# Kernel optimization log

Measured on AMD Instinct MI355X. Metric: run time of the kernel, lower is better.

Reference implementation:

```python
import math
import jax, jax.numpy as jnp
import numpy as np

B, C, F, W_FRAMES = 1, 8, 1024, 512
H = 16                      # num_heads
D = F // H                  # head dim = 64
ROPE_DIM = D // 2           # 32: only first half of head dim is rotated
EXP = 4                     # ffn expansion
EPS = 1e-5
MAX_FREQ = 10.0             # rotary-embedding-torch default


def frame_norm(x, g, b):
    # LayerNorm over the feature axis (axis=2) of (b, c, F, w)
    mu = jnp.mean(x, axis=2, keepdims=True)
    var = jnp.mean(jnp.square(x - mu), axis=2, keepdims=True)
    xn = (x - mu) * jax.lax.rsqrt(var + EPS)
    return xn * g[None, None, :, None] + b[None, None, :, None]


def mc_linear(x, w_pw):
    # per-channel pointwise linear: out[b,c,f,w] = sum_g W[c,f,g] x[b,c,g,w]
    return jnp.einsum('bcgw,cfg->bcfw', x, w_pw)


def apply_rope(t, freqs_seq):
    # t: (b, c, H, w, d); freqs_seq: (w, rot_dim)
    rot_dim = freqs_seq.shape[-1]
    t_rot, t_pass = t[..., :rot_dim], t[..., rot_dim:]
    cos, sin = jnp.cos(freqs_seq), jnp.sin(freqs_seq)
    x1, x2 = t_rot[..., 0::2], t_rot[..., 1::2]
    rh = jnp.stack([-x2, x1], axis=-1).reshape(t_rot.shape)  # interleaved rotate_half
    return jnp.concatenate([t_rot * cos + rh * sin, t_pass], axis=-1)


def attention(x, w_q, w_o, rope_freqs):
    b, c, f, w = x.shape
    # NOTE: source uses q_proj for q, k AND v (k_proj/v_proj unused)
    p = mc_linear(x, w_q)                                    # (b,c,F,w)
    t = p.transpose(0, 1, 3, 2).reshape(b, c, w, H, D).transpose(0, 1, 3, 2, 4)  # (b,c,H,w,d)
    pos = jnp.arange(w, dtype=t.dtype)
    freqs_seq = jnp.repeat(pos[:, None] * rope_freqs[None, :], 2, axis=-1)  # (w, rot_dim)
    q = apply_rope(t, freqs_seq)
    k = apply_rope(t, freqs_seq)
    v = t
    scores = jnp.einsum('bchqd,bchkd->bchqk', q, k) / math.sqrt(f)  # scaled by sqrt(features)!
    a = jax.nn.softmax(scores, axis=-1)
    o = jnp.einsum('bchqk,bchkd->bchqd', a, v)
    o = o.transpose(0, 1, 3, 2, 4).reshape(b, c, w, f).transpose(0, 1, 3, 2)  # (b,c,F,w)
    return mc_linear(o, w_o)


def setup_inputs() -> dict:
    key = jax.random.key(0)
    ks = jax.random.split(key, 8)
    s = 1.0 / math.sqrt(F)
    se = 1.0 / math.sqrt(F * EXP)
    x = jax.random.normal(ks[0], (B, C, F, W_FRAMES), dtype=jnp.float32)
    w_q = jax.random.uniform(ks[1], (C, F, F), jnp.float32, -s, s)
    w_o = jax.random.uniform(ks[2], (C, F, F), jnp.float32, -s, s)
    w1 = jax.random.uniform(ks[3], (C, F * EXP, F), jnp.float32, -s, s)
    w2 = jax.random.uniform(ks[4], (C, F, F * EXP), jnp.float32, -se, se)
    rope_freqs = jnp.linspace(1.0, MAX_FREQ / 2, ROPE_DIM // 2, dtype=jnp.float32) * math.pi
    return {
        'x': x,
        'norm1_g': jnp.ones((F,), jnp.float32), 'norm1_b': jnp.zeros((F,), jnp.float32),
        'w_q': w_q, 'w_o': w_o, 'rope_freqs': rope_freqs,
        'norm2_g': jnp.ones((F,), jnp.float32), 'norm2_b': jnp.zeros((F,), jnp.float32),
        'w1': w1, 'w2': w2,
    }


def reference(x, norm1_g, norm1_b, w_q, w_o, rope_freqs, norm2_g, norm2_b, w1, w2):
    # FrameTransformerEncoder, eval mode (dropout = identity)
    z = frame_norm(x, norm1_g, norm1_b)
    x = x + attention(z, w_q, w_o, rope_freqs)
    z = frame_norm(x, norm2_g, norm2_b)
    z = mc_linear(jax.nn.gelu(mc_linear(z, w1), approximate=False), w2)
    return x + z
```

## Files before the change

kernel.cpp:

```cpp
#include <hip/hip_runtime.h>
#include <math.h>

#define CC 8
#define FF 1024
#define WW 512
#define HH 16
#define DD 64
#define FE 4096
#define EPS_ 1e-5f

typedef __attribute__((ext_vector_type(8))) short bf16x8;
typedef __attribute__((ext_vector_type(4))) float f32x4;

static __device__ __forceinline__ unsigned short f2bf(float f) {
    unsigned u = __float_as_uint(f);
    u += 0x7fffu + ((u >> 16) & 1u);
    return (unsigned short)(u >> 16);
}
static __device__ __forceinline__ float bf2f(unsigned short h) {
    return __uint_as_float(((unsigned)h) << 16);
}
static __device__ __forceinline__ float gelu_exact(float v) {
    return 0.5f * v * (1.0f + erff(v * 0.70710678118654752f));
}
static __device__ __forceinline__ unsigned cvt_pk_bf16(float lo, float hi) {
    unsigned r;
    asm("v_cvt_pk_bf16_f32 %0, %1, %2" : "=v"(r) : "v"(lo), "v"(hi));
    return r;
}

typedef const __attribute__((address_space(1))) unsigned int* gas_p;
typedef __attribute__((address_space(3))) unsigned int* las_p;
static __device__ __forceinline__ void gload_lds16(const void* g, void* l) {
    __builtin_amdgcn_global_load_lds((gas_p)g, (las_p)l, 16, 0, 0);
}

__global__ __launch_bounds__(256) void fn_stats_k(
    const float* __restrict__ x, float2* __restrict__ part)
{
    int c  = blockIdx.z;
    int w0 = blockIdx.x * 64;
    int f0 = blockIdx.y * 128;
    int t  = threadIdx.x, wl = t & 63, fg = t >> 6;
    const float* xc = x + (size_t)c * FF * WW;

    float s = 0.f, q = 0.f;
    #pragma unroll 8
    for (int i = 0; i < 32; i++) {
        int f = f0 + fg + 4 * i;
        float v = xc[(size_t)f * WW + w0 + wl];
        s += v; q += v * v;
    }
    __shared__ float ss[4][64], sq_[4][64];
    ss[fg][wl] = s; sq_[fg][wl] = q;
    __syncthreads();
    if (fg == 0) {
        float S = 0.f, Q = 0.f;
        #pragma unroll
        for (int j = 0; j < 4; j++) { S += ss[j][wl]; Q += sq_[j][wl]; }
        part[((size_t)c * WW + w0 + wl) * 8 + blockIdx.y] = make_float2(S, Q);
    }
}

__global__ __launch_bounds__(256) void fn_apply_k(
    const float* __restrict__ x, const float2* __restrict__ part,
    const float* __restrict__ g, const float* __restrict__ b,
    unsigned short* __restrict__ zt)
{
    int c  = blockIdx.z;
    int w0 = blockIdx.x * 64;
    int f0 = blockIdx.y * 64;
    int t  = threadIdx.x, wl = t & 63, fg = t >> 6;

    __shared__ float smu[64], srv[64];
    __shared__ float sT[64][65];

    if (t < 64) {
        float S = 0.f, Q = 0.f;
        #pragma unroll
        for (int fs = 0; fs < 8; fs++) {
            float2 v = part[((size_t)c * WW + w0 + t) * 8 + fs];
            S += v.x; Q += v.y;
        }
        float mu  = S * (1.f / FF);
        float var = Q * (1.f / FF) - mu * mu;
        smu[t] = mu;
        srv[t] = rsqrtf(var + EPS_);
    }
    const float* xc = x + (size_t)c * FF * WW;
    #pragma unroll
    for (int i = 0; i < 16; i++) {
        int fl = fg * 16 + i;
        sT[fl][wl] = xc[(size_t)(f0 + fl) * WW + w0 + wl];
    }
    __syncthreads();

    unsigned short* ztc = zt + (size_t)c * WW * FF;
    float gv = g[f0 + wl], bv = b[f0 + wl];
    #pragma unroll
    for (int i = 0; i < 16; i++) {
        int wr = fg * 16 + i;
        ztc[(size_t)(w0 + wr) * FF + f0 + wl] =
            f2bf((sT[wl][wr] - smu[wr]) * srv[wr] * gv + bv);
    }
}

template<int BM, int MINW>
__global__ __launch_bounds__(256, MINW) void gemm_v6_k(
    const float* __restrict__ A, const unsigned short* __restrict__ Bt,
    float* __restrict__ Outf, unsigned short* __restrict__ Outb,
    const float* __restrict__ Add, int M, int K, int mode)
{
    constexpr int L  = BM / 16;
    constexpr int MI = BM / 32;
    constexpr int AP = 72;

    int bid = blockIdx.x;
    int c   = bid & 7;
    int rem = bid >> 3;
    int nt  = rem & 3;
    int mt  = rem >> 2;
    int m0  = mt * BM, n0 = nt * 128;
    const float*          Ac = A  + (size_t)c * M * K;
    const unsigned short* Bc = Bt + ((size_t)c * 512 + n0) * K;

    __shared__ unsigned short sA[2][BM * AP];
    __shared__ unsigned short sB[2][128 * 64];

    int t    = threadIdx.x;
    int lane = t & 63;
    int wid  = t >> 6;
    int frl  = lane & 15, fgr = lane >> 4;
    int WM   = (wid >> 1) * (MI * 16);
    int WN   = (wid & 1) * 64;

    f32x4 acc[MI][4];
    #pragma unroll
    for (int i = 0; i < MI; i++)
        #pragma unroll
        for (int j = 0; j < 4; j++) acc[i][j] = (f32x4){0.f, 0.f, 0.f, 0.f};

    int arow = t >> 4;
    int acol = (t & 15) * 4;
    float4 ar[L];

    int bro   = lane >> 3;
    int bslot = (lane & 7) ^ bro;

    auto loadA = [&](int k0) {
        #pragma unroll
        for (int p = 0; p < L; p++)
            ar[p] = *reinterpret_cast<const float4*>(
                Ac + (size_t)(m0 + p * 16 + arow) * K + k0 + acol);
    };
    auto cvtWriteA = [&](int buf) {
        #pragma unroll
        for (int p = 0; p < L; p++) {
            uint2 u;
            u.x = cvt_pk_bf16(ar[p].x, ar[p].y);
            u.y = cvt_pk_bf16(ar[p].z, ar[p].w);
            *reinterpret_cast<uint2*>(&sA[buf][(p * 16 + arow) * AP + acol]) = u;
        }
    };
    auto stageB = [&](int buf, int k0) {
        #pragma unroll
        for (int r = 0; r < 4; r++) {
            int rbase = wid * 32 + r * 8;
            gload_lds16(Bc + (size_t)(rbase + bro) * K + k0 + bslot * 8,
                        &sB[buf][rbase * 64]);
        }
    };

    loadA(0);
    asm volatile("s_waitcnt vmcnt(0)" ::: "memory");
    cvtWriteA(0);
    stageB(0, 0);

    int NT = K >> 6;
    for (int kt = 0; kt < NT; ++kt) {
        int  cur  = kt & 1;
        bool more = (kt + 1 < NT);

        if (more) loadA((kt + 1) << 6);
        if (more) {
            if constexpr (BM == 128)
                asm volatile("s_waitcnt vmcnt(8)" ::: "memory");
            else
                asm volatile("s_waitcnt vmcnt(4)" ::: "memory");
        } else {
            asm volatile("s_waitcnt vmcnt(0)" ::: "memory");
        }
        asm volatile("s_waitcnt lgkmcnt(0)" ::: "memory");
        __builtin_amdgcn_sched_barrier(0);
        __builtin_amdgcn_s_barrier();

        if (more) stageB(cur ^ 1, (kt + 1) << 6);

        #pragma unroll
        for (int ks = 0; ks < 2; ks++) {
            bf16x8 af[MI], bfv[4];
            #pragma unroll
            for (int mi = 0; mi < MI; mi++)
                af[mi] = *reinterpret_cast<const bf16x8*>(
                    &sA[cur][(WM + mi * 16 + frl) * AP + ks * 32 + fgr * 8]);
            #pragma unroll
            for (int ni = 0; ni < 4; ni++) {
                int row  = WN + ni * 16 + frl;
                int slot = ((ks << 2) | fgr) ^ (frl & 7);
                bfv[ni] = *reinterpret_cast<const bf16x8*>(
                    &sB[cur][row * 64 + slot * 8]);
            }
            #pragma unroll
            for (int mi = 0; mi < MI; mi++)
                #pragma unroll
                for (int ni = 0; ni < 4; ni++)
                    acc[mi][ni] = __builtin_amdgcn_mfma_f32_16x16x32_bf16(
                        af[mi], bfv[ni], acc[mi][ni], 0, 0, 0);
        }

        if (more) {
            asm volatile("s_waitcnt vmcnt(4)" ::: "memory");
            __builtin_amdgcn_sched_barrier(0);
            cvtWriteA(cur ^ 1);
        }
    }

    if (mode == 1) {
        #pragma unroll
        for (int mi = 0; mi < MI; mi++)
            #pragma unroll
            for (int ni = 0; ni < 4; ni++) {
                int mrow = m0 + WM + mi * 16 + fgr * 4;
                int ncol = n0 + WN + ni * 16 + frl;
                #pragma unroll
                for (int r = 0; r < 4; r++) {
                    size_t o = ((size_t)c * M + mrow + r) * 512 + ncol;
                    Outf[o] = acc[mi][ni][r] + Add[o];
                }
            }
    } else {
        bool gel = (mode == 2);
        #pragma unroll
        for (int mi = 0; mi < MI; mi++)
            #pragma unroll
            for (int ni = 0; ni < 4; ni++) {
                f32x4 v = acc[mi][ni];
                if (gel) {
                    v[0] = gelu_exact(v[0]); v[1] = gelu_exact(v[1]);
                    v[2] = gelu_exact(v[2]); v[3] = gelu_exact(v[3]);
                }
                int mrow = m0 + WM + mi * 16 + fgr * 4;
                int ncol = n0 + WN + ni * 16 + frl;
                ushort4 h;
                h.x = f2bf(v[0]); h.y = f2bf(v[1]);
                h.z = f2bf(v[2]); h.w = f2bf(v[3]);
                *reinterpret_cast<ushort4*>(
                    &Outb[((size_t)c * 512 + ncol) * M + mrow]) = h;
            }
    }
}

__global__ __launch_bounds__(256, 2) void gemm_w1big_k(
    const float* __restrict__ A, const unsigned short* __restrict__ Bt,
    unsigned short* __restrict__ Outb, int M, int K)
{
    constexpr int L  = 4;
    constexpr int G  = 4;
    constexpr int AP = 40;

    int bid = blockIdx.x;
    int c   = bid & 7;
    int rem = bid >> 3;
    int nt  = rem & 1;
    int mt  = rem >> 1;
    int m0  = mt * 128, n0 = nt * 256;
    const float*          Ac = A  + (size_t)c * M * K;
    const unsigned short* Bc = Bt + ((size_t)c * 512 + n0) * K;

    __shared__ unsigned short sA[2][128 * AP];
    __shared__ unsigned short sB[2][256 * 32];

    int t    = threadIdx.x;
    int lane = t & 63;
    int wid  = t >> 6;
    int frl  = lane & 15, fgr = lane >> 4;
    int WM   = (wid >> 1) * 64;
    int WN   = (wid & 1) * 128;

    f32x4 acc[4][8];
    #pragma unroll
    for (int i = 0; i < 4; i++)
        #pragma unroll
        for (int j = 0; j < 8; j++) acc[i][j] = (f32x4){0.f, 0.f, 0.f, 0.f};

    int arow = t >> 3;
    int acol = (t & 7) * 4;
    float4 ar[L];

    int bro   = lane >> 2;
    int bslot = (lane & 3) ^ (bro & 3);

    auto loadA = [&](int k0) {
        #pragma unroll
        for (int p = 0; p < L; p++)
            ar[p] = *reinterpret_cast<const float4*>(
                Ac + (size_t)(m0 + p * 32 + arow) * K + k0 + acol);
    };
    auto cvtWriteA = [&](int buf) {
        #pragma unroll
        for (int p = 0; p < L; p++) {
            uint2 u;
            u.x = cvt_pk_bf16(ar[p].x, ar[p].y);
            u.y = cvt_pk_bf16(ar[p].z, ar[p].w);
            *reinterpret_cast<uint2*>(&sA[buf][(p * 32 + arow) * AP + acol]) = u;
        }
    };
    auto stageB = [&](int buf, int k0) {
        #pragma unroll
        for (int r = 0; r < G; r++) {
            int rbase = wid * 64 + r * 16;
            gload_lds16(Bc + (size_t)(rbase + bro) * K + k0 + bslot * 8,
                        &sB[buf][rbase * 32]);
        }
    };

    loadA(0);
    asm volatile("s_waitcnt vmcnt(0)" ::: "memory");
    cvtWriteA(0);
    stageB(0, 0);

    int NT = K >> 5;
    for (int kt = 0; kt < NT; ++kt) {
        int  cur  = kt & 1;
        bool more = (kt + 1 < NT);

        if (more) loadA((kt + 1) << 5);
        if (more)
            asm volatile("s_waitcnt vmcnt(4)" ::: "memory");
        else
            asm volatile("s_waitcnt vmcnt(0)" ::: "memory");
        asm volatile("s_waitcnt lgkmcnt(0)" ::: "memory");
        __builtin_amdgcn_sched_barrier(0);
        __builtin_amdgcn_s_barrier();

        if (more) stageB(cur ^ 1, (kt + 1) << 5);

        {
            bf16x8 af[4], bfv[8];
            #pragma unroll
            for (int mi = 0; mi < 4; mi++)
                af[mi] = *reinterpret_cast<const bf16x8*>(
                    &sA[cur][(WM + mi * 16 + frl) * AP + fgr * 8]);
            #pragma unroll
            for (int ni = 0; ni < 8; ni++) {
                int row  = WN + ni * 16 + frl;
                int slot = fgr ^ (row & 3);
                bfv[ni] = *reinterpret_cast<const bf16x8*>(
                    &sB[cur][row * 32 + slot * 8]);
            }
            #pragma unroll
            for (int mi = 0; mi < 4; mi++)
                #pragma unroll
                for (int ni = 0; ni < 8; ni++)
                    acc[mi][ni] = __builtin_amdgcn_mfma_f32_16x16x32_bf16(
                        af[mi], bfv[ni], acc[mi][ni], 0, 0, 0);
        }

        if (more) {
            asm volatile("s_waitcnt vmcnt(4)" ::: "memory");
            __builtin_amdgcn_sched_barrier(0);
            cvtWriteA(cur ^ 1);
        }
    }

    #pragma unroll
    for (int mi = 0; mi < 4; mi++)
        #pragma unroll
        for (int ni = 0; ni < 8; ni++) {
            f32x4 v = acc[mi][ni];
            v[0] = gelu_exact(v[0]); v[1] = gelu_exact(v[1]);
            v[2] = gelu_exact(v[2]); v[3] = gelu_exact(v[3]);
            int mrow = m0 + WM + mi * 16 + fgr * 4;
            int ncol = n0 + WN + ni * 16 + frl;
            ushort4 h;
            h.x = f2bf(v[0]); h.y = f2bf(v[1]);
            h.z = f2bf(v[2]); h.w = f2bf(v[3]);
            *reinterpret_cast<ushort4*>(
                &Outb[((size_t)c * 512 + ncol) * M + mrow]) = h;
        }
}

__global__ __launch_bounds__(256) void attn_mfma_k(
    const unsigned short* __restrict__ pt, const float* __restrict__ fr,
    unsigned short* __restrict__ ot)
{
    int ch = blockIdx.y;
    int c  = ch >> 4, h = ch & 15;
    int q0 = blockIdx.x * 64;
    int t  = threadIdx.x;
    int lane = t & 63;
    int wid  = t >> 6;
    int frl  = lane & 15, fgr = lane >> 4;

    const unsigned short* base = pt + (size_t)c * WW * FF + h * DD;

    __shared__ unsigned short Qs[64 * 72];
    __shared__ unsigned short Ks[64 * 72];
    __shared__ unsigned short Vt[64 * 72];
    __shared__ unsigned short Ps[4 * 16 * 72];

    {
        int kr = t >> 3, d0 = (t & 7) * 8;
        #pragma unroll
        for (int r = 0; r < 2; r++) {
            int row = kr + r * 32;
            int w   = q0 + row;
            bf16x8 v = *reinterpret_cast<const bf16x8*>(&base[(size_t)w * FF + d0]);
            bf16x8 o;
            if (d0 < 32) {
                #pragma unroll
                for (int j = 0; j < 8; j += 2) {
                    float x1 = bf2f((unsigned short)v[j]);
                    float x2 = bf2f((unsigned short)v[j + 1]);
                    float sn, cs;
                    __sincosf((float)w * fr[(d0 + j) >> 1], &sn, &cs);
                    o[j]     = (short)f2bf(x1 * cs - x2 * sn);
                    o[j + 1] = (short)f2bf(x2 * cs + x1 * sn);
                }
            } else o = v;
            *reinterpret_cast<bf16x8*>(&Qs[row * 72 + d0]) = o;
        }
    }

    f32x4 oacc[4];
    float m_[4], l_[4];
    #pragma unroll
    for (int i = 0; i < 4; i++) {
        oacc[i] = (f32x4){0.f, 0.f, 0.f, 0.f};
        m_[i] = -1e30f; l_[i] = 0.f;
    }
    unsigned short* myP = &Ps[wid * 16 * 72];
    int wq0 = wid * 16;

    for (int k0 = 0; k0 < WW; k0 += 64) {
        __syncthreads();
        {
            int kr = t >> 3, d0 = (t & 7) * 8;
            #pragma unroll
            for (int r = 0; r < 2; r++) {
                int row = kr + r * 32;
                int w   = k0 + row;
                bf16x8 v = *reinterpret_cast<const bf16x8*>(&base[(size_t)w * FF + d0]);
                bf16x8 o;
                if (d0 < 32) {
                    #pragma unroll
                    for (int j = 0; j < 8; j += 2) {
                        float x1 = bf2f((unsigned short)v[j]);
                        float x2 = bf2f((unsigned short)v[j + 1]);
                        float sn, cs;
                        __sincosf((float)w * fr[(d0 + j) >> 1], &sn, &cs);
                        o[j]     = (short)f2bf(x1 * cs - x2 * sn);
                        o[j + 1] = (short)f2bf(x2 * cs + x1 * sn);
                    }
                } else o = v;
                *reinterpret_cast<bf16x8*>(&Ks[row * 72 + d0]) = o;
            }
        }
        {
            int d  = t & 63;
            int kb = (t >> 6) * 8;
            #pragma unroll
            for (int r = 0; r < 2; r++) {
                int kk = kb + r * 32;
                bf16x8 o;
                #pragma unroll
                for (int j = 0; j < 8; j++)
                    o[j] = (short)base[(size_t)(k0 + kk + j) * FF + d];
                *reinterpret_cast<bf16x8*>(&Vt[d * 72 + kk]) = o;
            }
        }
        __syncthreads();

        f32x4 s[4];
        #pragma unroll
        for (int nt = 0; nt < 4; nt++) s[nt] = (f32x4){0.f, 0.f, 0.f, 0.f};
        bf16x8 aq0 = *reinterpret_cast<const bf16x8*>(&Qs[(wq0 + frl) * 72 + fgr * 8]);
        bf16x8 aq1 = *reinterpret_cast<const bf16x8*>(&Qs[(wq0 + frl) * 72 + 32 + fgr * 8]);
        #pragma unroll
        for (int nt = 0; nt < 4; nt++) {
            bf16x8 b0 = *reinterpret_cast<const bf16x8*>(&Ks[(nt * 16 + frl) * 72 + fgr * 8]);
            bf16x8 b1 = *reinterpret_cast<const bf16x8*>(&Ks[(nt * 16 + frl) * 72 + 32 + fgr * 8]);
            s[nt] = __builtin_amdgcn_mfma_f32_16x16x32_bf16(aq0, b0, s[nt], 0, 0, 0);
            s[nt] = __builtin_amdgcn_mfma_f32_16x16x32_bf16(aq1, b1, s[nt], 0, 0, 0);
        }

        #pragma unroll
        for (int r = 0; r < 4; r++) {
            float sv[4];
            #pragma unroll
            for (int nt = 0; nt < 4; nt++) sv[nt] = s[nt][r] * (1.f / 32.f);
            float mx = fmaxf(fmaxf(sv[0], sv[1]), fmaxf(sv[2], sv[3]));
            mx = fmaxf(mx, __shfl_xor(mx, 1, 64));
            mx = fmaxf(mx, __shfl_xor(mx, 2, 64));
            mx = fmaxf(mx, __shfl_xor(mx, 4, 64));
            mx = fmaxf(mx, __shfl_xor(mx, 8, 64));
            float mn    = fmaxf(m_[r], mx);
            float scale = __expf(m_[r] - mn);
            float rs = 0.f;
            #pragma unroll
            for (int nt = 0; nt < 4; nt++) {
                float p = __expf(sv[nt] - mn);
                myP[(fgr * 4 + r) * 72 + nt * 16 + frl] = f2bf(p);
                rs += p;
            }
            rs += __shfl_xor(rs, 1, 64);
            rs += __shfl_xor(rs, 2, 64);
            rs += __shfl_xor(rs, 4, 64);
            rs += __shfl_xor(rs, 8, 64);
            l_[r] = l_[r] * scale + rs;
            m_[r] = mn;
            #pragma unroll
            for (int dt = 0; dt < 4; dt++) oacc[dt][r] *= scale;
        }

        bf16x8 ap0 = *reinterpret_cast<const bf16x8*>(&myP[frl * 72 + fgr * 8]);
        bf16x8 ap1 = *reinterpret_cast<const bf16x8*>(&myP[frl * 72 + 32 + fgr * 8]);
        #pragma unroll
        for (int dt = 0; dt < 4; dt++) {
            bf16x8 b0 = *reinterpret_cast<const bf16x8*>(&Vt[(dt * 16 + frl) * 72 + fgr * 8]);
            bf16x8 b1 = *reinterpret_cast<const bf16x8*>(&Vt[(dt * 16 + frl) * 72 + 32 + fgr * 8]);
            oacc[dt] = __builtin_amdgcn_mfma_f32_16x16x32_bf16(ap0, b0, oacc[dt], 0, 0, 0);
            oacc[dt] = __builtin_amdgcn_mfma_f32_16x16x32_bf16(ap1, b1, oacc[dt], 0, 0, 0);
        }
    }

    unsigned short* ob = ot + (size_t)c * WW * FF + h * DD;
    #pragma unroll
    for (int r = 0; r < 4; r++) {
        float inv = 1.f / l_[r];
        int w = q0 + wq0 + fgr * 4 + r;
        #pragma unroll
        for (int dt = 0; dt < 4; dt++)
            ob[(size_t)w * FF + dt * 16 + frl] = f2bf(oacc[dt][r] * inv);
    }
}

extern "C" void kernel_launch(void* const* d_in, const int* in_sizes, int n_in,
                              void* d_out, int out_size, void* d_ws, size_t ws_size,
                              hipStream_t stream)
{
    const float* x  = (const float*)d_in[0];
    const float* g1 = (const float*)d_in[1];
    const float* b1 = (const float*)d_in[2];
    const float* wq = (const float*)d_in[3];
    const float* wo = (const float*)d_in[4];
    const float* fr = (const float*)d_in[5];
    const float* g2 = (const float*)d_in[6];
    const float* b2 = (const float*)d_in[7];
    const float* w1 = (const float*)d_in[8];
    const float* w2 = (const float*)d_in[9];

    const size_t SZ = (size_t)CC * FF * WW;
    char* wsb = (char*)d_ws;
    unsigned short* zt  = (unsigned short*)(wsb);
    unsigned short* ptb = (unsigned short*)(wsb + 2 * SZ);
    unsigned short* otb = (unsigned short*)(wsb + 4 * SZ);
    float*          x2  = (float*)        (wsb + 6 * SZ);
    unsigned short* h1t = (unsigned short*)(wsb + 10 * SZ);
    float2*         prt = (float2*)       (wsb + 18 * SZ);

    dim3 b256(256);
    dim3 gst(WW / 64, FF / 128, CC);
    dim3 gap(WW / 64, FF / 64, CC);

    fn_stats_k<<<gst, b256, 0, stream>>>(x, prt);
    fn_apply_k<<<gap, b256, 0, stream>>>(x, prt, g1, b1, zt);
    gemm_v6_k<64, 3><<<dim3(512), b256, 0, stream>>>(
        wq, zt, nullptr, ptb, nullptr, FF, FF, 0);
    attn_mfma_k<<<dim3(WW / 64, CC * HH), b256, 0, stream>>>(ptb, fr, otb);
    gemm_v6_k<64, 3><<<dim3(512), b256, 0, stream>>>(
        wo, otb, x2, nullptr, x, FF, FF, 1);
    fn_stats_k<<<gst, b256, 0, stream>>>(x2, prt);
    fn_apply_k<<<gap, b256, 0, stream>>>(x2, prt, g2, b2, zt);
    gemm_w1big_k<<<dim3(512), b256, 0, stream>>>(w1, zt, h1t, FE, FF);
    gemm_v6_k<64, 3><<<dim3(512), b256, 0, stream>>>(
        w2, h1t, (float*)d_out, nullptr, x2, FF, FE, 1);
}
```

Baseline: 259.9 us.

## Replace block-shared FFN GEMMs with barrier-free per-wave tiled GEMM kernel

The FFN GEMM kernels (w1 with GELU, and w2 with residual add) are replaced by a templated kernel in which each wave owns private LDS buffers for its A and B tiles. This removes the block-wide s_barrier per k-step and adds deeper A register prefetch, two tiles ahead. The w2 GEMM now uses this kernel in place of gemm_v6_k. The tradeoff is that B tiles are no longer shared across waves, so each wave loads its own B and global and LDS traffic rises. Smaller per-wave tiles also lower MFMA reuse per load.

```diff
diff --git a/kernel.cpp b/kernel.cpp
--- a/kernel.cpp
+++ b/kernel.cpp
@@ -260,134 +260,158 @@
     }
 }
 
-__global__ __launch_bounds__(256, 2) void gemm_w1big_k(
+template<int MI, int NI, int MODE>
+__global__ __launch_bounds__(256, 2) void gemm_wfree_k(
     const float* __restrict__ A, const unsigned short* __restrict__ Bt,
-    unsigned short* __restrict__ Outb, int M, int K)
+    float* __restrict__ Outf, unsigned short* __restrict__ Outb,
+    const float* __restrict__ Add, int M, int K)
 {
-    constexpr int L  = 4;
-    constexpr int G  = 4;
-    constexpr int AP = 40;
+    constexpr int R   = MI * 16;
+    constexpr int BN  = NI * 16;
+    constexpr int L   = R / 8;
+    constexpr int G   = NI;
+    constexpr int NTn = 512 / BN;
+    constexpr int LPR = 64 / R;
+    constexpr int FPL = 32 / LPR;
 
     int bid = blockIdx.x;
     int c   = bid & 7;
     int rem = bid >> 3;
-    int nt  = rem & 1;
-    int mt  = rem >> 1;
-    int m0  = mt * 128, n0 = nt * 256;
-    const float*          Ac = A  + (size_t)c * M * K;
-    const unsigned short* Bc = Bt + ((size_t)c * 512 + n0) * K;
-
-    __shared__ unsigned short sA[2][128 * AP];
-    __shared__ unsigned short sB[2][256 * 32];
+    int nt  = rem & (NTn - 1);
+    int mtb = rem / NTn;
 
     int t    = threadIdx.x;
     int lane = t & 63;
     int wid  = t >> 6;
+    int m0w  = (mtb * 4 + wid) * R;
+    int n0   = nt * BN;
+
+    const float*          Ac = A  + (size_t)c * M * K;
+    const unsigned short* Bc = Bt + ((size_t)c * 512 + n0) * K;
+
+    __shared__ unsigned short sB[4][BN * 32];
+    __shared__ unsigned short sA[4][2][R * 40];
+    unsigned short* sBw = sB[wid];
+
     int frl  = lane & 15, fgr = lane >> 4;
-    int WM   = (wid >> 1) * 64;
-    int WN   = (wid & 1) * 128;
-
-    f32x4 acc[4][8];
+    int arow = lane / LPR, asub = lane % LPR;
+    int bro  = lane >> 2;
+    int bslot = (lane & 3) ^ (bro & 3);
+
+    f32x4 acc[MI][NI];
     #pragma unroll
-    for (int i = 0; i < 4; i++)
-        #pragma unroll
-        for (int j = 0; j < 8; j++) acc[i][j] = (f32x4){0.f, 0.f, 0.f, 0.f};
-
-    int arow = t >> 3;
-    int acol = (t & 7) * 4;
-    float4 ar[L];
-
-    int bro   = lane >> 2;
-    int bslot = (lane & 3) ^ (bro & 3);
-
-    auto loadA = [&](int k0) {
+    for (int i = 0; i < MI; i++)
+        #pragma unroll
+        for (int j = 0; j < NI; j++) acc[i][j] = (f32x4){0.f, 0.f, 0.f, 0.f};
+
+    float4 ar0[L], ar1[L];
+
+    auto loadAinto = [&](int k0, float4 (&ar)[L]) {
         #pragma unroll
         for (int p = 0; p < L; p++)
             ar[p] = *reinterpret_cast<const float4*>(
-                Ac + (size_t)(m0 + p * 32 + arow) * K + k0 + acol);
+                Ac + (size_t)(m0w + arow) * K + k0 + asub * FPL + p * 4);
     };
-    auto cvtWriteA = [&](int buf) {
+    auto cvtWriteA = [&](int buf, float4 (&ar)[L]) {
         #pragma unroll
         for (int p = 0; p < L; p++) {
             uint2 u;
             u.x = cvt_pk_bf16(ar[p].x, ar[p].y);
             u.y = cvt_pk_bf16(ar[p].z, ar[p].w);
-            *reinterpret_cast<uint2*>(&sA[buf][(p * 32 + arow) * AP + acol]) = u;
+            *reinterpret_cast<uint2*>(
+                &sA[wid][buf][arow * 40 + asub * FPL + p * 4]) = u;
         }
     };
-    auto stageB = [&](int buf, int k0) {
-        #pragma unroll
-        for (int r = 0; r < G; r++) {
-            int rbase = wid * 64 + r * 16;
-            gload_lds16(Bc + (size_t)(rbase + bro) * K + k0 + bslot * 8,
-                        &sB[buf][rbase * 32]);
-        }
+    auto stageB = [&](int k0) {
+        #pragma unroll
+        for (int r = 0; r < G; r++)
+            gload_lds16(Bc + (size_t)(r * 16 + bro) * K + k0 + bslot * 8,
+                        &sBw[r * 512]);
     };
 
-    loadA(0);
+    int NT = K >> 5;
+
+    loadAinto(0, ar0);
     asm volatile("s_waitcnt vmcnt(0)" ::: "memory");
-    cvtWriteA(0);
-    stageB(0, 0);
-
-    int NT = K >> 5;
-    for (int kt = 0; kt < NT; ++kt) {
-        int  cur  = kt & 1;
-        bool more = (kt + 1 < NT);
-
-        if (more) loadA((kt + 1) << 5);
-        if (more)
-            asm volatile("s_waitcnt vmcnt(4)" ::: "memory");
-        else
-            asm volatile("s_waitcnt vmcnt(0)" ::: "memory");
+    __builtin_amdgcn_sched_barrier(0);
+    cvtWriteA(0, ar0);
+    stageB(0);
+    loadAinto(32, ar1);
+
+    auto body = [&](int kt, float4 (&arW)[L], float4 (&arR)[L]) {
+        bool more1 = (kt + 1 < NT), more2 = (kt + 2 < NT);
+        int  cur   = kt & 1;
+
+        if (more1) asm volatile("s_waitcnt vmcnt(%0)" :: "i"(L) : "memory");
+        else       asm volatile("s_waitcnt vmcnt(0)" ::: "memory");
+        __builtin_amdgcn_sched_barrier(0);
+
+        bf16x8 af[MI], bfv[NI];
+        #pragma unroll
+        for (int mi = 0; mi < MI; mi++)
+            af[mi] = *reinterpret_cast<const bf16x8*>(
+                &sA[wid][cur][(mi * 16 + frl) * 40 + fgr * 8]);
+        #pragma unroll
+        for (int ni = 0; ni < NI; ni++) {
+            int row  = ni * 16 + frl;
+            int slot = fgr ^ (row & 3);
+            bfv[ni] = *reinterpret_cast<const bf16x8*>(
+                &sBw[row * 32 + slot * 8]);
+        }
         asm volatile("s_waitcnt lgkmcnt(0)" ::: "memory");
         __builtin_amdgcn_sched_barrier(0);
-        __builtin_amdgcn_s_barrier();
-
-        if (more) stageB(cur ^ 1, (kt + 1) << 5);
-
-        {
-            bf16x8 af[4], bfv[8];
-            #pragma unroll
-            for (int mi = 0; mi < 4; mi++)
-                af[mi] = *reinterpret_cast<const bf16x8*>(
-                    &sA[cur][(WM + mi * 16 + frl) * AP + fgr * 8]);
-            #pragma unroll
-            for (int ni = 0; ni < 8; ni++) {
-                int row  = WN + ni * 16 + frl;
-                int slot = fgr ^ (row & 3);
-                bfv[ni] = *reinterpret_cast<const bf16x8*>(
-                    &sB[cur][row * 32 + slot * 8]);
-            }
-            #pragma unroll
-            for (int mi = 0; mi < 4; mi++)
+
+        if (more1) {
+            stageB((kt + 1) << 5);
+            asm volatile("s_waitcnt vmcnt(%0)" :: "i"(G) : "memory");
+            __builtin_amdgcn_sched_barrier(0);
+            cvtWriteA(cur ^ 1, arR);
+            if (more2) loadAinto((kt + 2) << 5, arW);
+        }
+
+        #pragma unroll
+        for (int mi = 0; mi < MI; mi++)
+            #pragma unroll
+            for (int ni = 0; ni < NI; ni++)
+                acc[mi][ni] = __builtin_amdgcn_mfma_f32_16x16x32_bf16(
+                    af[mi], bfv[ni], acc[mi][ni], 0, 0, 0);
+    };
+
+    for (int kt = 0; kt < NT; kt += 2) {
+        body(kt,     ar0, ar1);
+        body(kt + 1, ar1, ar0);
+    }
+
+    if constexpr (MODE == 1) {
+        #pragma unroll
+        for (int mi = 0; mi < MI; mi++)
+            #pragma unroll
+            for (int ni = 0; ni < NI; ni++) {
+                int mrow = m0w + mi * 16 + fgr * 4;
+                int ncol = n0 + ni * 16 + frl;
                 #pragma unroll
-                for (int ni = 0; ni < 8; ni++)
-                    acc[mi][ni] = __builtin_amdgcn_mfma_f32_16x16x32_bf16(
-                        af[mi], bfv[ni], acc[mi][ni], 0, 0, 0);
-        }
-
-        if (more) {
-            asm volatile("s_waitcnt vmcnt(4)" ::: "memory");
-            __builtin_amdgcn_sched_barrier(0);
-            cvtWriteA(cur ^ 1);
-        }
-    }
-
-    #pragma unroll
-    for (int mi = 0; mi < 4; mi++)
-        #pragma unroll
-        for (int ni = 0; ni < 8; ni++) {
-            f32x4 v = acc[mi][ni];
-            v[0] = gelu_exact(v[0]); v[1] = gelu_exact(v[1]);
-            v[2] = gelu_exact(v[2]); v[3] = gelu_exact(v[3]);
-            int mrow = m0 + WM + mi * 16 + fgr * 4;
-            int ncol = n0 + WN + ni * 16 + frl;
-            ushort4 h;
-            h.x = f2bf(v[0]); h.y = f2bf(v[1]);
-            h.z = f2bf(v[2]); h.w = f2bf(v[3]);
-            *reinterpret_cast<ushort4*>(
-                &Outb[((size_t)c * 512 + ncol) * M + mrow]) = h;
-        }
+                for (int r = 0; r < 4; r++) {
+                    size_t o = ((size_t)c * M + mrow + r) * 512 + ncol;
+                    Outf[o] = acc[mi][ni][r] + Add[o];
+                }
+            }
+    } else {
+        #pragma unroll
+        for (int mi = 0; mi < MI; mi++)
+            #pragma unroll
+            for (int ni = 0; ni < NI; ni++) {
+                f32x4 v = acc[mi][ni];
+                v[0] = gelu_exact(v[0]); v[1] = gelu_exact(v[1]);
+                v[2] = gelu_exact(v[2]); v[3] = gelu_exact(v[3]);
+                int mrow = m0w + mi * 16 + fgr * 4;
+                int ncol = n0 + ni * 16 + frl;
+                ushort4 h;
+                h.x = f2bf(v[0]); h.y = f2bf(v[1]);
+                h.z = f2bf(v[2]); h.w = f2bf(v[3]);
+                *reinterpret_cast<ushort4*>(
+                    &Outb[((size_t)c * 512 + ncol) * M + mrow]) = h;
+            }
+    }
 }
 
 __global__ __launch_bounds__(256) void attn_mfma_k(
@@ -582,7 +606,8 @@
         wo, otb, x2, nullptr, x, FF, FF, 1);
     fn_stats_k<<<gst, b256, 0, stream>>>(x2, prt);
     fn_apply_k<<<gap, b256, 0, stream>>>(x2, prt, g2, b2, zt);
-    gemm_w1big_k<<<dim3(512), b256, 0, stream>>>(w1, zt, h1t, FE, FF);
-    gemm_v6_k<64, 3><<<dim3(512), b256, 0, stream>>>(
-        w2, h1t, (float*)d_out, nullptr, x2, FF, FE, 1);
-}
+    gemm_wfree_k<2, 8, 2><<<dim3(1024), b256, 0, stream>>>(
+        w1, zt, nullptr, h1t, nullptr, FE, FF);
+    gemm_wfree_k<2, 4, 1><<<dim3(512), b256, 0, stream>>>(
+        w2, h1t, (float*)d_out, nullptr, x2, FF, FE);
+}
```

Result: slower. 371.2 us (+42.8%).
